# Kernel optimization log

Measured on AMD Instinct MI355X. Metric: run time of the kernel, lower is better.

The kernel has to match this reference:

```python
import jax, jax.numpy as jnp
import numpy as np

# ---- fixed encoding config (mirrors PermutoEncoding __init__ args) ----
POS_DIM = 3
DP1 = POS_DIM + 1                 # simplex has pos_dim+1 vertices
CAPACITY = 262144                 # hash table size per level (2^18)
NR_LEVELS = 24
NR_FEAT = 2
N_POINTS = 262144
SCALES = np.geomspace(1.0, 1e-4, NR_LEVELS).astype(np.float32)  # coarse -> fine
# permutohedral elevation scale factors (Adams et al.): 1/sqrt((i+1)(i+2)) * invStdDev
INV_STD_DEV = DP1 * np.sqrt(2.0 / 3.0)
SCALE_FACTOR = (INV_STD_DEV / np.sqrt((np.arange(POS_DIM) + 1.0) * (np.arange(POS_DIM) + 2.0))).astype(np.float32)
PRIMES = np.array([2654435761, 805459861, 3674653429], dtype=np.uint32)


def setup_inputs() -> dict:
    key = jax.random.key(0)
    k1, k2, k3 = jax.random.split(key, 3)
    positions = jax.random.uniform(k1, (N_POINTS, POS_DIM), jnp.float32)
    # matches torch.randn(capacity, L, F)*1e-5 permuted to [L, C, F]
    lattice_values = jax.random.normal(k2, (NR_LEVELS, CAPACITY, NR_FEAT), jnp.float32) * 1e-5
    random_shift = jax.random.normal(k3, (NR_LEVELS, POS_DIM), jnp.float32) * 10.0
    anneal_window = jnp.ones((NR_LEVELS,), jnp.float32)
    return {"positions": positions, "lattice_values": lattice_values,
            "random_shift": random_shift, "anneal_window": anneal_window}


def _permuto_encode(positions, lattice_values, random_shift, anneal_window):
    scales = jnp.asarray(SCALES)
    sf = jnp.asarray(SCALE_FACTOR)
    # per-level scaled + shifted positions: [L, N, d]
    p = positions[None, :, :] / scales[:, None, None] + random_shift[:, None, :]
    cf = p * sf                                              # [L,N,d]
    # elevate onto hyperplane H_d in R^{d+1}
    rev_cumsum = jnp.cumsum(cf[..., ::-1], axis=-1)[..., ::-1]   # S[k] = sum_{j>=k} cf[j]
    e0 = rev_cumsum[..., :1]                                 # elevated[0] = sum cf
    S = jnp.concatenate([rev_cumsum[..., 1:], jnp.zeros_like(e0)], axis=-1)
    irange = jnp.arange(1, DP1, dtype=cf.dtype)
    elevated = jnp.concatenate([e0, S - irange * cf], axis=-1)  # [L,N,d+1]

    # nearest zero-colored lattice point (round each coord to multiple of d+1)
    rem0 = jnp.round(elevated / DP1) * DP1                   # [L,N,d+1]
    dvec = elevated - rem0
    # rank[i] = #{j>i : d_i < d_j} + #{j<i : d_j >= d_i}
    less = dvec[..., :, None] < dvec[..., None, :]           # [.., i, j] = d_i < d_j
    idxr = jnp.arange(DP1)
    j_gt_i = idxr[:, None] < idxr[None, :]
    j_lt_i = idxr[:, None] > idxr[None, :]
    rank = (less & j_gt_i).sum(-1).astype(jnp.int32) \
         + ((~jnp.swapaxes(less, -1, -2)) & j_lt_i).sum(-1).astype(jnp.int32)
    s = jnp.round(rem0.sum(-1) / DP1).astype(jnp.int32)      # [L,N]
    rank = rank + s[..., None]
    lo = rank < 0
    rank = rank + lo.astype(jnp.int32) * DP1
    rem0 = rem0 + lo.astype(rem0.dtype) * DP1
    hi = rank > POS_DIM
    rank = rank - hi.astype(jnp.int32) * DP1
    rem0 = rem0 - hi.astype(rem0.dtype) * DP1

    # barycentric weights (size d+2, wrapped)
    delta = (elevated - rem0) / DP1
    oh = jax.nn.one_hot(POS_DIM - rank, DP1 + 1, dtype=delta.dtype) \
       - jax.nn.one_hot(DP1 - rank, DP1 + 1, dtype=delta.dtype)
    b = jnp.einsum('...i,...ij->...j', delta, oh)            # [L,N,d+2]
    w0 = b[..., 0] + 1.0 + b[..., DP1]
    weights = jnp.concatenate([w0[..., None], b[..., 1:DP1]], axis=-1)  # [L,N,d+1]

    # simplex vertex keys (first d coords), one per remainder r=0..d
    r = jnp.arange(DP1, dtype=jnp.int32)                     # vertex axis
    rem0i = jnp.round(rem0).astype(jnp.int32)
    keys = rem0i[..., None, :POS_DIM] + r[:, None] \
         - DP1 * (rank[..., None, :POS_DIM] > POS_DIM - r[:, None]).astype(jnp.int32)  # [L,N,d+1,d]

    # hash keys into the per-level table
    ku = keys.astype(jnp.uint32) * jnp.asarray(PRIMES)[None, None, None, :]
    h = ku[..., 0] ^ ku[..., 1] ^ ku[..., 2]
    idx = (h % jnp.uint32(CAPACITY)).astype(jnp.int32)       # [L,N,d+1]

    # gather per-level features and blend with barycentric weights
    vals = jax.vmap(lambda tbl, ix: tbl[ix])(lattice_values, idx)   # [L,N,d+1,F]
    sliced = jnp.einsum('lnv,lnvf->lnf', weights, vals) * anneal_window[:, None, None]
    # (L,F,N).permute(2,0,1).reshape(N,-1) == [N, L, F] -> [N, L*F]
    return jnp.transpose(sliced, (1, 0, 2)).reshape(positions.shape[0], -1)


def reference(positions, lattice_values, random_shift, anneal_window):
    return _permuto_encode(positions, lattice_values, random_shift, anneal_window)
```

## Files before the change

kernel.cpp:

```cpp
#include <hip/hip_runtime.h>
#include <math.h>

#define N_LEVELS 24
#define CAPACITY 262144u
#define CAP_MASK 0x3FFFFu

struct ScaleArg { float s[N_LEVELS]; };

struct Prep {
    float w0, w1, w2, w3;
    unsigned i0, i1, i2, i3;
};

__device__ __forceinline__ Prep permuto_prep(
    float p0, float p1, float p2,
    float scale, float s0, float s1, float s2)
{
#pragma clang fp contract(off)
    const float sf0 = 2.3094010767585034f;
    const float sf1 = 1.3333333333333335f;
    const float sf2 = 0.9428090415820634f;

    const float q0 = p0 / scale + s0;
    const float q1 = p1 / scale + s1;
    const float q2 = p2 / scale + s2;
    const float cf0 = q0 * sf0;
    const float cf1 = q1 * sf1;
    const float cf2 = q2 * sf2;

    const float rc1 = cf2 + cf1;
    const float el0 = rc1 + cf0;
    const float el1 = rc1 - cf0;
    const float el2 = cf2 - 2.0f * cf1;
    const float el3 = 0.0f - 3.0f * cf2;

    float r0 = rintf(el0 * 0.25f) * 4.0f;
    float r1 = rintf(el1 * 0.25f) * 4.0f;
    float r2 = rintf(el2 * 0.25f) * 4.0f;
    float r3 = rintf(el3 * 0.25f) * 4.0f;

    const float d0 = el0 - r0;
    const float d1 = el1 - r1;
    const float d2 = el2 - r2;
    const float d3 = el3 - r3;

    int k0 = 0, k1 = 0, k2 = 0, k3 = 0;
    if (d0 < d1) k0++; else k1++;
    if (d0 < d2) k0++; else k2++;
    if (d0 < d3) k0++; else k3++;
    if (d1 < d2) k1++; else k2++;
    if (d1 < d3) k1++; else k3++;
    if (d2 < d3) k2++; else k3++;

    const int s = (int)rintf((((r0 + r1) + r2) + r3) * 0.25f);
    k0 += s; k1 += s; k2 += s; k3 += s;

    if (k0 < 0) { k0 += 4; r0 += 4.0f; } else if (k0 > 3) { k0 -= 4; r0 -= 4.0f; }
    if (k1 < 0) { k1 += 4; r1 += 4.0f; } else if (k1 > 3) { k1 -= 4; r1 -= 4.0f; }
    if (k2 < 0) { k2 += 4; r2 += 4.0f; } else if (k2 > 3) { k2 -= 4; r2 -= 4.0f; }
    if (k3 < 0) { k3 += 4; r3 += 4.0f; } else if (k3 > 3) { k3 -= 4; r3 -= 4.0f; }

    const float dl0 = (el0 - r0) * 0.25f;
    const float dl1 = (el1 - r1) * 0.25f;
    const float dl2 = (el2 - r2) * 0.25f;
    const float dl3 = (el3 - r3) * 0.25f;

    const float g0 = (k0 == 0 ? dl0 : 0.0f) + (k1 == 0 ? dl1 : 0.0f) + (k2 == 0 ? dl2 : 0.0f) + (k3 == 0 ? dl3 : 0.0f);
    const float g1 = (k0 == 1 ? dl0 : 0.0f) + (k1 == 1 ? dl1 : 0.0f) + (k2 == 1 ? dl2 : 0.0f) + (k3 == 1 ? dl3 : 0.0f);
    const float g2 = (k0 == 2 ? dl0 : 0.0f) + (k1 == 2 ? dl1 : 0.0f) + (k2 == 2 ? dl2 : 0.0f) + (k3 == 2 ? dl3 : 0.0f);
    const float g3 = (k0 == 3 ? dl0 : 0.0f) + (k1 == 3 ? dl1 : 0.0f) + (k2 == 3 ? dl2 : 0.0f) + (k3 == 3 ? dl3 : 0.0f);

    Prep out;
    out.w0 = g3 + 1.0f - g0;
    out.w1 = g2 - g3;
    out.w2 = g1 - g2;
    out.w3 = g0 - g1;

    const int i0 = (int)r0;
    const int i1 = (int)r1;
    const int i2 = (int)r2;

    unsigned idx[4];
#pragma unroll
    for (int r = 0; r < 4; ++r) {
        const int key0 = i0 + r - ((k0 > 3 - r) ? 4 : 0);
        const int key1 = i1 + r - ((k1 > 3 - r) ? 4 : 0);
        const int key2 = i2 + r - ((k2 > 3 - r) ? 4 : 0);
        const unsigned hsh = (unsigned)key0 * 2654435761u
                           ^ (unsigned)key1 * 805459861u
                           ^ (unsigned)key2 * 3674653429u;
        idx[r] = hsh & CAP_MASK;
    }
    out.i0 = idx[0]; out.i1 = idx[1]; out.i2 = idx[2]; out.i3 = idx[3];
    return out;
}

__global__ __launch_bounds__(256)
void permuto_gather(const float* __restrict__ pos,
                    const float* __restrict__ lattice,
                    const float* __restrict__ rshift,
                    const float* __restrict__ anneal,
                    float2* __restrict__ ws,
                    ScaleArg sc, int npts, int balanced, int chunksPerLevel)
{
#pragma clang fp contract(off)
    int level, chunk;
    const int xcd = blockIdx.x & 7;
    if (balanced) {
        const int slot = blockIdx.x >> 3;
        if (slot < 1024)      { level = 8 + xcd;  chunk = slot; }
        else if (slot < 2048) { level = 16 + xcd; chunk = slot - 1024; }
        else {
            const int s = slot - 2048;
            level = s & 7;
            chunk = (s & ~7) | xcd;
        }
    } else {
        const int j = blockIdx.x >> 3;
        const int phase = j / chunksPerLevel;
        chunk = j - phase * chunksPerLevel;
        level = phase * 8 + xcd;
    }

    const int n = chunk * 256 + threadIdx.x;
    if (n >= npts) return;

    const float scale = sc.s[level];
    const float s0 = rshift[level * 3 + 0];
    const float s1 = rshift[level * 3 + 1];
    const float s2 = rshift[level * 3 + 2];
    const float a  = anneal[level];

    const float p0 = pos[n * 3 + 0];
    const float p1 = pos[n * 3 + 1];
    const float p2 = pos[n * 3 + 2];

    const float2* __restrict__ tab = (const float2*)lattice + (size_t)level * CAPACITY;

    Prep pr = permuto_prep(p0, p1, p2, scale, s0, s1, s2);

    const float2 v0 = tab[pr.i0];
    const float2 v1 = tab[pr.i1];
    const float2 v2 = tab[pr.i2];
    const float2 v3 = tab[pr.i3];

    const float ax = pr.w0 * v0.x + pr.w1 * v1.x + pr.w2 * v2.x + pr.w3 * v3.x;
    const float ay = pr.w0 * v0.y + pr.w1 * v1.y + pr.w2 * v2.y + pr.w3 * v3.y;

    ws[(size_t)level * npts + n] = make_float2(ax * a, ay * a);
}

__global__ __launch_bounds__(256)
void permuto_transpose(const float2* __restrict__ ws,
                       float4* __restrict__ out, int npts)
{
    __shared__ float2 sh[N_LEVELS][257];
    const int t = threadIdx.x;
    const int pbase = blockIdx.x * 256;
    const int valid = npts - pbase;

    if (valid >= 256) {
#pragma unroll
        for (int l = 0; l < N_LEVELS; ++l)
            sh[l][t] = ws[(size_t)l * npts + pbase + t];
        __syncthreads();

        float4* o = out + (size_t)pbase * 12;
#pragma unroll
        for (int s = 0; s < 12; ++s) {
            const int q = s * 256 + t;
            const int p = q / 12;
            const int j = q - p * 12;
            const float2 va = sh[2 * j][p];
            const float2 vb = sh[2 * j + 1][p];
            o[q] = make_float4(va.x, va.y, vb.x, vb.y);
        }
    } else {
        if (t < valid) {
            const int n = pbase + t;
            float4* o = out + (size_t)n * 12;
#pragma unroll
            for (int j = 0; j < 12; ++j) {
                const float2 va = ws[(size_t)(2 * j) * npts + n];
                const float2 vb = ws[(size_t)(2 * j + 1) * npts + n];
                o[j] = make_float4(va.x, va.y, vb.x, vb.y);
            }
        }
    }
}

__global__ __launch_bounds__(256)
void permuto_mono(const float* __restrict__ pos,
                  const float* __restrict__ lattice,
                  const float* __restrict__ rshift,
                  const float* __restrict__ anneal,
                  float* __restrict__ out,
                  ScaleArg sc, int npts)
{
#pragma clang fp contract(off)
    __shared__ float sh_shift[N_LEVELS][3];
    __shared__ float sh_ann[N_LEVELS];
    const int tid = threadIdx.x;
    if (tid < N_LEVELS) {
        sh_shift[tid][0] = rshift[tid * 3 + 0];
        sh_shift[tid][1] = rshift[tid * 3 + 1];
        sh_shift[tid][2] = rshift[tid * 3 + 2];
        sh_ann[tid] = anneal[tid];
    }
    __syncthreads();

    const int n = blockIdx.x * 256 + tid;
    if (n >= npts) return;
    const float p0 = pos[n * 3 + 0];
    const float p1 = pos[n * 3 + 1];
    const float p2 = pos[n * 3 + 2];
    float2* outv = (float2*)out + (size_t)n * N_LEVELS;
    for (int l = 0; l < N_LEVELS; ++l) {
        const float2* tab = (const float2*)lattice + (size_t)l * CAPACITY;
        Prep pr = permuto_prep(p0, p1, p2, sc.s[l],
                               sh_shift[l][0], sh_shift[l][1], sh_shift[l][2]);
        float2 v0 = tab[pr.i0], v1 = tab[pr.i1], v2 = tab[pr.i2], v3 = tab[pr.i3];
        float ax = pr.w0 * v0.x + pr.w1 * v1.x + pr.w2 * v2.x + pr.w3 * v3.x;
        float ay = pr.w0 * v0.y + pr.w1 * v1.y + pr.w2 * v2.y + pr.w3 * v3.y;
        outv[l] = make_float2(ax * sh_ann[l], ay * sh_ann[l]);
    }
}

extern "C" void kernel_launch(void* const* d_in, const int* in_sizes, int n_in,
                              void* d_out, int out_size, void* d_ws, size_t ws_size,
                              hipStream_t stream) {
    const float* pos     = (const float*)d_in[0];
    const float* lattice = (const float*)d_in[1];
    const float* rshift  = (const float*)d_in[2];
    const float* anneal  = (const float*)d_in[3];
    const int npts = in_sizes[0] / 3;

    ScaleArg sc;
    for (int i = 0; i < N_LEVELS; ++i)
        sc.s[i] = (float)pow(10.0, (double)i * (-4.0 / 23.0));
    sc.s[0] = 1.0f;
    sc.s[N_LEVELS - 1] = 1e-4f;

    const size_t ws_need = (size_t)N_LEVELS * (size_t)npts * sizeof(float2);
    if (ws_size >= ws_need) {
        const int C = (npts + 255) / 256;
        if (C == 1024) {
            permuto_gather<<<8 * 3072, 256, 0, stream>>>(
                pos, lattice, rshift, anneal, (float2*)d_ws, sc, npts, 1, C);
        } else {
            permuto_gather<<<8 * 3 * C, 256, 0, stream>>>(
                pos, lattice, rshift, anneal, (float2*)d_ws, sc, npts, 0, C);
        }
        const int blocks2 = (npts + 255) / 256;
        permuto_transpose<<<blocks2, 256, 0, stream>>>(
            (const float2*)d_ws, (float4*)d_out, npts);
    } else {
        const int blocks = (npts + 255) / 256;
        permuto_mono<<<blocks, 256, 0, stream>>>(
            pos, lattice, rshift, anneal, (float*)d_out, sc, npts);
    }
}
```

Measured before the change: 197.5 us.

## Fuse per-level gather and transpose into one kernel over 8-level groups

Replaces the two-kernel scheme (per-level gather into a workspace, then a transpose kernel) with one fused kernel. Each block handles 512 points across a group of 8 levels, stages results in shared memory, and writes 64-byte slices of the interleaved output directly. This drops the workspace round trip (write plus reread of the full intermediate) and one launch. The cost is less parallelism per level, more registers for two points per thread, and an XCD mapping that no longer keeps one level's table per XCD L2.

New measurement: 224.4 us. +13.6%, slower.

```diff
diff --git a/kernel.cpp b/kernel.cpp
--- a/kernel.cpp
+++ b/kernel.cpp
@@ -4,6 +4,8 @@
 #define N_LEVELS 24
 #define CAPACITY 262144u
 #define CAP_MASK 0x3FFFFu
+#define PTS 512
+#define LPG 8
 
 struct ScaleArg { float s[N_LEVELS]; };
 
@@ -96,133 +98,86 @@
 }
 
 __global__ __launch_bounds__(256)
-void permuto_gather(const float* __restrict__ pos,
-                    const float* __restrict__ lattice,
-                    const float* __restrict__ rshift,
-                    const float* __restrict__ anneal,
-                    float2* __restrict__ ws,
-                    ScaleArg sc, int npts, int balanced, int chunksPerLevel)
+void permuto_fused(const float* __restrict__ pos,
+                   const float* __restrict__ lattice,
+                   const float* __restrict__ rshift,
+                   const float* __restrict__ anneal,
+                   float4* __restrict__ out,
+                   ScaleArg sc, int npts, int balanced, int chunks)
 {
 #pragma clang fp contract(off)
-    int level, chunk;
-    const int xcd = blockIdx.x & 7;
+    int group, chunk;
     if (balanced) {
+        const int xcd  = blockIdx.x & 7;
         const int slot = blockIdx.x >> 3;
-        if (slot < 1024)      { level = 8 + xcd;  chunk = slot; }
-        else if (slot < 2048) { level = 16 + xcd; chunk = slot - 1024; }
-        else {
-            const int s = slot - 2048;
-            level = s & 7;
-            chunk = (s & ~7) | xcd;
+        if (slot < 128) {
+            group = 1 + (xcd >> 2);
+            chunk = (slot << 2) | (xcd & 3);
+        } else {
+            group = 0;
+            chunk = ((slot - 128) << 3) | xcd;
         }
     } else {
-        const int j = blockIdx.x >> 3;
-        const int phase = j / chunksPerLevel;
-        chunk = j - phase * chunksPerLevel;
-        level = phase * 8 + xcd;
-    }
-
-    const int n = chunk * 256 + threadIdx.x;
-    if (n >= npts) return;
-
-    const float scale = sc.s[level];
-    const float s0 = rshift[level * 3 + 0];
-    const float s1 = rshift[level * 3 + 1];
-    const float s2 = rshift[level * 3 + 2];
-    const float a  = anneal[level];
-
-    const float p0 = pos[n * 3 + 0];
-    const float p1 = pos[n * 3 + 1];
-    const float p2 = pos[n * 3 + 2];
-
-    const float2* __restrict__ tab = (const float2*)lattice + (size_t)level * CAPACITY;
-
-    Prep pr = permuto_prep(p0, p1, p2, scale, s0, s1, s2);
-
-    const float2 v0 = tab[pr.i0];
-    const float2 v1 = tab[pr.i1];
-    const float2 v2 = tab[pr.i2];
-    const float2 v3 = tab[pr.i3];
-
-    const float ax = pr.w0 * v0.x + pr.w1 * v1.x + pr.w2 * v2.x + pr.w3 * v3.x;
-    const float ay = pr.w0 * v0.y + pr.w1 * v1.y + pr.w2 * v2.y + pr.w3 * v3.y;
-
-    ws[(size_t)level * npts + n] = make_float2(ax * a, ay * a);
-}
-
-__global__ __launch_bounds__(256)
-void permuto_transpose(const float2* __restrict__ ws,
-                       float4* __restrict__ out, int npts)
-{
-    __shared__ float2 sh[N_LEVELS][257];
+        group = blockIdx.x / chunks;
+        chunk = blockIdx.x - group * chunks;
+    }
+
     const int t = threadIdx.x;
-    const int pbase = blockIdx.x * 256;
-    const int valid = npts - pbase;
-
-    if (valid >= 256) {
+    const int pbase = chunk * PTS;
+
+    __shared__ float2 sh[LPG][PTS];
+
+    const int n0 = pbase + t;
+    const int n1 = pbase + t + 256;
+    float p0x = 0.f, p0y = 0.f, p0z = 0.f;
+    float p1x = 0.f, p1y = 0.f, p1z = 0.f;
+    if (n0 < npts) { p0x = pos[n0 * 3 + 0]; p0y = pos[n0 * 3 + 1]; p0z = pos[n0 * 3 + 2]; }
+    if (n1 < npts) { p1x = pos[n1 * 3 + 0]; p1y = pos[n1 * 3 + 1]; p1z = pos[n1 * 3 + 2]; }
+
 #pragma unroll
-        for (int l = 0; l < N_LEVELS; ++l)
-            sh[l][t] = ws[(size_t)l * npts + pbase + t];
-        __syncthreads();
-
-        float4* o = out + (size_t)pbase * 12;
+    for (int l = 0; l < LPG; ++l) {
+        const int level = group * LPG + l;
+        const float scale = sc.s[level];
+        const float s0 = rshift[level * 3 + 0];
+        const float s1 = rshift[level * 3 + 1];
+        const float s2 = rshift[level * 3 + 2];
+        const float a  = anneal[level];
+        const float2* __restrict__ tab =
+            (const float2*)lattice + (size_t)level * CAPACITY;
+
+        const Prep A = permuto_prep(p0x, p0y, p0z, scale, s0, s1, s2);
+        const Prep B = permuto_prep(p1x, p1y, p1z, scale, s0, s1, s2);
+
+        const float2 va0 = tab[A.i0];
+        const float2 va1 = tab[A.i1];
+        const float2 va2 = tab[A.i2];
+        const float2 va3 = tab[A.i3];
+        const float2 vb0 = tab[B.i0];
+        const float2 vb1 = tab[B.i1];
+        const float2 vb2 = tab[B.i2];
+        const float2 vb3 = tab[B.i3];
+
+        const float ax = A.w0 * va0.x + A.w1 * va1.x + A.w2 * va2.x + A.w3 * va3.x;
+        const float ay = A.w0 * va0.y + A.w1 * va1.y + A.w2 * va2.y + A.w3 * va3.y;
+        const float bx = B.w0 * vb0.x + B.w1 * vb1.x + B.w2 * vb2.x + B.w3 * vb3.x;
+        const float by = B.w0 * vb0.y + B.w1 * vb1.y + B.w2 * vb2.y + B.w3 * vb3.y;
+
+        sh[l][t]       = make_float2(ax * a, ay * a);
+        sh[l][t + 256] = make_float2(bx * a, by * a);
+    }
+    __syncthreads();
+
 #pragma unroll
-        for (int s = 0; s < 12; ++s) {
-            const int q = s * 256 + t;
-            const int p = q / 12;
-            const int j = q - p * 12;
+    for (int k = 0; k < 8; ++k) {
+        const int q = k * 256 + t;
+        const int p = q >> 2;
+        const int j = q & 3;
+        const int n = pbase + p;
+        if (n < npts) {
             const float2 va = sh[2 * j][p];
             const float2 vb = sh[2 * j + 1][p];
-            o[q] = make_float4(va.x, va.y, vb.x, vb.y);
+            out[(size_t)n * 12 + group * 4 + j] = make_float4(va.x, va.y, vb.x, vb.y);
         }
-    } else {
-        if (t < valid) {
-            const int n = pbase + t;
-            float4* o = out + (size_t)n * 12;
-#pragma unroll
-            for (int j = 0; j < 12; ++j) {
-                const float2 va = ws[(size_t)(2 * j) * npts + n];
-                const float2 vb = ws[(size_t)(2 * j + 1) * npts + n];
-                o[j] = make_float4(va.x, va.y, vb.x, vb.y);
-            }
-        }
-    }
-}
-
-__global__ __launch_bounds__(256)
-void permuto_mono(const float* __restrict__ pos,
-                  const float* __restrict__ lattice,
-                  const float* __restrict__ rshift,
-                  const float* __restrict__ anneal,
-                  float* __restrict__ out,
-                  ScaleArg sc, int npts)
-{
-#pragma clang fp contract(off)
-    __shared__ float sh_shift[N_LEVELS][3];
-    __shared__ float sh_ann[N_LEVELS];
-    const int tid = threadIdx.x;
-    if (tid < N_LEVELS) {
-        sh_shift[tid][0] = rshift[tid * 3 + 0];
-        sh_shift[tid][1] = rshift[tid * 3 + 1];
-        sh_shift[tid][2] = rshift[tid * 3 + 2];
-        sh_ann[tid] = anneal[tid];
-    }
-    __syncthreads();
-
-    const int n = blockIdx.x * 256 + tid;
-    if (n >= npts) return;
-    const float p0 = pos[n * 3 + 0];
-    const float p1 = pos[n * 3 + 1];
-    const float p2 = pos[n * 3 + 2];
-    float2* outv = (float2*)out + (size_t)n * N_LEVELS;
-    for (int l = 0; l < N_LEVELS; ++l) {
-        const float2* tab = (const float2*)lattice + (size_t)l * CAPACITY;
-        Prep pr = permuto_prep(p0, p1, p2, sc.s[l],
-                               sh_shift[l][0], sh_shift[l][1], sh_shift[l][2]);
-        float2 v0 = tab[pr.i0], v1 = tab[pr.i1], v2 = tab[pr.i2], v3 = tab[pr.i3];
-        float ax = pr.w0 * v0.x + pr.w1 * v1.x + pr.w2 * v2.x + pr.w3 * v3.x;
-        float ay = pr.w0 * v0.y + pr.w1 * v1.y + pr.w2 * v2.y + pr.w3 * v3.y;
-        outv[l] = make_float2(ax * sh_ann[l], ay * sh_ann[l]);
     }
 }
 
@@ -241,22 +196,8 @@
     sc.s[0] = 1.0f;
     sc.s[N_LEVELS - 1] = 1e-4f;
 
-    const size_t ws_need = (size_t)N_LEVELS * (size_t)npts * sizeof(float2);
-    if (ws_size >= ws_need) {
-        const int C = (npts + 255) / 256;
-        if (C == 1024) {
-            permuto_gather<<<8 * 3072, 256, 0, stream>>>(
-                pos, lattice, rshift, anneal, (float2*)d_ws, sc, npts, 1, C);
-        } else {
-            permuto_gather<<<8 * 3 * C, 256, 0, stream>>>(
-                pos, lattice, rshift, anneal, (float2*)d_ws, sc, npts, 0, C);
-        }
-        const int blocks2 = (npts + 255) / 256;
-        permuto_transpose<<<blocks2, 256, 0, stream>>>(
-            (const float2*)d_ws, (float4*)d_out, npts);
-    } else {
-        const int blocks = (npts + 255) / 256;
-        permuto_mono<<<blocks, 256, 0, stream>>>(
-            pos, lattice, rshift, anneal, (float*)d_out, sc, npts);
-    }
+    const int C = (npts + PTS - 1) / PTS;
+    const int balanced = (C == 512) ? 1 : 0;
+    permuto_fused<<<3 * C, 256, 0, stream>>>(
+        pos, lattice, rshift, anneal, (float4*)d_out, sc, npts, balanced, C);
 }
```
